# Performance work log

Measured on AMD Instinct MI355X. Metric: run time of the kernel, lower is better.

The kernel has to match this reference:

```python
import jax, jax.numpy as jnp
import numpy as np

N, E, B, T, F, H, O = 50000, 800000, 16, 4, 128, 128, 128
LEAKY = 0.2  # PyG GATConv negative_slope default


def setup_inputs() -> dict:
    key = jax.random.key(0)
    ks = jax.random.split(key, 12)
    s = 0.05
    return {
        "x": jax.random.normal(ks[0], (T, N, F), jnp.float32),
        "edge_index": jax.random.randint(ks[1], (2, E), 0, N, dtype=jnp.int32),
        "batch_idx": jnp.sort(jax.random.randint(ks[2], (N,), 0, B, dtype=jnp.int32)),
        "W1": jax.random.normal(ks[3], (F, H), jnp.float32) * s,
        "att_src1": jax.random.normal(ks[4], (H,), jnp.float32) * s,
        "att_dst1": jax.random.normal(ks[5], (H,), jnp.float32) * s,
        "b1": jnp.zeros((H,), jnp.float32),
        "W2": jax.random.normal(ks[6], (H, O), jnp.float32) * s,
        "att_src2": jax.random.normal(ks[7], (O,), jnp.float32) * s,
        "att_dst2": jax.random.normal(ks[8], (O,), jnp.float32) * s,
        "b2": jnp.zeros((O,), jnp.float32),
    }


def gat_layer(h, src, dst, W, a_src, a_dst, b):
    # PyG GATConv, heads=1, concat=False, self-loops already appended.
    h = h @ W                                  # [N, out]
    alpha_s = h @ a_src                        # [N]
    alpha_d = h @ a_dst                        # [N]
    e = alpha_s[src] + alpha_d[dst]            # [E']
    e = jnp.where(e > 0, e, LEAKY * e)         # leaky_relu
    # softmax over incoming edges of each destination node (every node has a self-loop)
    m = jax.ops.segment_max(e, dst, num_segments=N)
    ex = jnp.exp(e - m[dst])
    z = jax.ops.segment_sum(ex, dst, num_segments=N)
    alpha = ex / z[dst]                        # [E']
    out = jax.ops.segment_sum(alpha[:, None] * h[src], dst, num_segments=N)
    return out + b


def reference(x, edge_index, batch_idx, W1, att_src1, att_dst1, b1, W2, att_src2, att_dst2, b2):
    loops = jnp.arange(N, dtype=edge_index.dtype)
    src = jnp.concatenate([edge_index[0], loops])  # add_self_loops (PyG default)
    dst = jnp.concatenate([edge_index[1], loops])
    ones = jnp.ones((N, 1), jnp.float32)
    cnt = jax.ops.segment_sum(ones, batch_idx, num_segments=B)  # [B,1]

    def per_snapshot(xt):
        h = gat_layer(xt, src, dst, W1, att_src1, att_dst1, b1)
        h = jax.nn.relu(h)                     # inter-layer ReLU (dropout=0, eval)
        h = gat_layer(h, src, dst, W2, att_src2, att_dst2, b2)
        return jax.ops.segment_sum(h, batch_idx, num_segments=B) / cnt  # mean pool [B,O]

    reps = jax.vmap(per_snapshot)(x)           # [T, B, O]
    return jnp.transpose(reps, (1, 0, 2))      # [B, T, O]
```

## Files before the change

kernel.cpp:

```cpp
#include <hip/hip_runtime.h>
#include <hip/hip_bf16.h>

#define LEAKY 0.2f

typedef __attribute__((ext_vector_type(8))) short bf16x8;
typedef __attribute__((ext_vector_type(4))) float f32x4;
typedef __attribute__((ext_vector_type(2))) float f32x2;


__global__ __launch_bounds__(256) void k_init(int* cnt, int* bstart, int* hist, int n, int nb) {
    int i = blockIdx.x * 256 + threadIdx.x;
    if (i < n) cnt[i] = 1;
    if (i < nb) bstart[i] = n;
    if (i < 32) hist[i] = 0;
}

__global__ __launch_bounds__(256) void k_count(const int* __restrict__ dst, int* cnt, int e,
                                               const int* __restrict__ bidx, int* bstart, int n) {
    int i = blockIdx.x * 256 + threadIdx.x;
    if (i < e) atomicAdd(&cnt[dst[i]], 1);
    if (i < n) {
        int b = bidx[i];
        if (i == 0 || bidx[i - 1] != b) atomicMin(&bstart[b], i);
    }
}

__device__ inline int block_incl_scan(int v, int* lds) {
    int lane = threadIdx.x & 63, wid = threadIdx.x >> 6;
    int s = v;
#pragma unroll
    for (int o = 1; o < 64; o <<= 1) { int t = __shfl_up(s, o); if (lane >= o) s += t; }
    if (lane == 63) lds[wid] = s;
    __syncthreads();
    int add = 0;
#pragma unroll
    for (int ww = 0; ww < 3; ++ww) if (ww < wid) add += lds[ww];
    return s + add;
}

__global__ __launch_bounds__(256) void k_scanA(const int* __restrict__ cnt, int* bsum, int n) {
    __shared__ int lds[4];
    int i = blockIdx.x * 256 + threadIdx.x;
    int v = (i < n) ? ((cnt[i] + 7) & ~7) : 0;
    int s = block_incl_scan(v, lds);
    if (threadIdx.x == 255) bsum[blockIdx.x] = s;
}

__global__ __launch_bounds__(256) void k_scanB(int* bsum, int* boff, int nb,
                                               int* bstart, int n, int nbatch) {
    __shared__ int lds[4];
    int i = threadIdx.x;
    int v = (i < nb) ? bsum[i] : 0;
    int s = block_incl_scan(v, lds);
    if (i < nb) boff[i] = s - v;
    if (i == 0) {
        bstart[nbatch] = n;
        for (int b = nbatch - 1; b >= 0; --b)
            if (bstart[b] == n) bstart[b] = bstart[b + 1];
    }
}

__global__ __launch_bounds__(256) void k_scanC(const int* __restrict__ cnt, const int* __restrict__ boff,
                                               int* row_ptr, int* csr, int* cursor, int* hist, int n) {
    __shared__ int lds[4];
    __shared__ int lh[32];
    int tid = threadIdx.x;
    if (tid < 32) lh[tid] = 0;
    int i = blockIdx.x * 256 + tid;
    int v = (i < n) ? ((cnt[i] + 7) & ~7) : 0;
    int s = block_incl_scan(v, lds) + boff[blockIdx.x];
    __syncthreads();
    if (i < n) {
        int excl = s - v;
        row_ptr[i + 1] = s;
        csr[excl] = i;
        cursor[i] = excl + 1;
        atomicAdd(&lh[min(v >> 3, 31)], 1);
    }
    if (i == 0) row_ptr[0] = 0;
    __syncthreads();
    if (tid < 32 && lh[tid]) atomicAdd(&hist[tid], lh[tid]);
}

__global__ __launch_bounds__(256) void k_scatter(const int* __restrict__ src, const int* __restrict__ dst,
                                                 int* cursor, int* csr, int e) {
    int i = blockIdx.x * 256 + threadIdx.x;
    if (i < e) { int p = atomicAdd(&cursor[dst[i]], 1); csr[p] = src[i]; }
}

__global__ void k_bscan(const int* __restrict__ hist, int* bcur) {
    int run = 0;
    for (int b = 0; b < 32; ++b) { bcur[b] = run; run += hist[b]; }
}

__global__ __launch_bounds__(256) void k_pad(const int* __restrict__ row_ptr, const int* __restrict__ cursor,
                                             int* csr, int* bcur, int* perm, int n) {
    __shared__ int lh[32];
    __shared__ int lbase[32];
    int tid = threadIdx.x;
    if (tid < 32) lh[tid] = 0;
    __syncthreads();
    int i = blockIdx.x * 256 + tid;
    int bkt = 0, lpos = 0, b0 = 0, p = 0, e = 0;
    if (i < n) {
        b0 = row_ptr[i]; p = cursor[i]; e = row_ptr[i + 1];
        bkt = min((e - b0) >> 3, 31);
        lpos = atomicAdd(&lh[bkt], 1);
    }
    __syncthreads();
    if (tid < 32 && lh[tid]) lbase[tid] = atomicAdd(&bcur[tid], lh[tid]);
    __syncthreads();
    if (i < n) {
        perm[lbase[bkt] + lpos] = i;
        int v = i | 0x80000000;
        for (; p < e; ++p) csr[p] = v;
    }
}

__device__ inline unsigned short bf16r(float x) {
    unsigned int u = __float_as_uint(x);
    u += 0x7fffu + ((u >> 16) & 1u);
    return (unsigned short)(u >> 16);
}

__device__ inline unsigned int bfpair(float lo, float hi) {
    unsigned int ul = __float_as_uint(lo); ul += 0x7fffu + ((ul >> 16) & 1u);
    unsigned int uh = __float_as_uint(hi); uh += 0x7fffu + ((uh >> 16) & 1u);
    return (ul >> 16) | (uh & 0xffff0000u);
}

__global__ __launch_bounds__(256) void k_prep(const float* __restrict__ W1, unsigned short* __restrict__ wt1g,
                                              const float* __restrict__ W2, unsigned short* __restrict__ wt2g) {
    int bi = blockIdx.x;
    const float* W = (bi < 64) ? W1 : W2;
    unsigned short* wtg = (bi < 64) ? wt1g : wt2g;
    int idx = (bi & 63) * 256 + threadIdx.x;
    int k = idx >> 7, n = idx & 127;
    int kg = k >> 3, kr = k & 7;
    wtg[(n * 16 + (kg ^ (n & 15))) * 8 + kr] = bf16r(W[k * 128 + n]);
}

template <bool ABF16>
__global__ __launch_bounds__(256) void k_gemm_mfma(
    const void* __restrict__ Asrc, const unsigned short* __restrict__ wtg,
    const float* __restrict__ asrc, const float* __restrict__ adst,
    unsigned char* __restrict__ hq, float* __restrict__ vas, float* __restrict__ vad,
    int nrows)
{
    __shared__ unsigned short Wt[128 * 128];
    int tid = threadIdx.x;
    int lane = tid & 63, wv = tid >> 6;
    int row0 = blockIdx.x * 64;
    int c0 = lane & 15, g = lane >> 4;

    int rA = min(row0 + wv * 16 + c0, nrows - 1);

    bf16x8 af[4];
    uint4 stg[8];
    {
        const uint4* s4 = (const uint4*)wtg;
#pragma unroll
        for (int i = 0; i < 8; ++i) stg[i] = s4[tid + i * 256];
    }
    if (ABF16) {
#pragma unroll
        for (int ks = 0; ks < 4; ++ks)
            af[ks] = *(const bf16x8*)((const unsigned short*)Asrc + (size_t)rA * 128 + ks * 32 + g * 8);
    } else {
        float4 raw[4][2];
#pragma unroll
        for (int ks = 0; ks < 4; ++ks) {
            const float4* ap = (const float4*)((const float*)Asrc + (size_t)rA * 128 + ks * 32 + g * 8);
            raw[ks][0] = ap[0];
            raw[ks][1] = ap[1];
        }
#pragma unroll
        for (int ks = 0; ks < 4; ++ks) {
            float4 f0 = raw[ks][0], f1 = raw[ks][1];
            uint4 p = make_uint4(bfpair(f0.x, f0.y), bfpair(f0.z, f0.w),
                                 bfpair(f1.x, f1.y), bfpair(f1.z, f1.w));
            af[ks] = *(bf16x8*)&p;
        }
    }
    {
        uint4* d4 = (uint4*)Wt;
#pragma unroll
        for (int i = 0; i < 8; ++i) d4[tid + i * 256] = stg[i];
    }
    __syncthreads();

    f32x4 acc[8];
#pragma unroll
    for (int ni = 0; ni < 8; ++ni)
#pragma unroll
        for (int q = 0; q < 4; ++q) acc[ni][q] = 0.f;

#pragma unroll
    for (int ks = 0; ks < 4; ++ks) {
        int kgbase = ks * 4;
        bf16x8 bfr[8];
#pragma unroll
        for (int ni = 0; ni < 8; ++ni) {
            int n = ni * 16 + c0;
            bfr[ni] = *(const bf16x8*)&Wt[(n * 16 + ((kgbase + g) ^ c0)) * 8];
        }
#pragma unroll
        for (int ni = 0; ni < 8; ++ni)
            acc[ni] = __builtin_amdgcn_mfma_f32_16x16x32_bf16(bfr[ni], af[ks], acc[ni], 0, 0, 0);
    }

    float4 as4[8], ad4[8];
#pragma unroll
    for (int ni = 0; ni < 8; ++ni) {
        as4[ni] = *(const float4*)&asrc[ni * 16 + g * 4];
        ad4[ni] = *(const float4*)&adst[ni * 16 + g * 4];
    }
    {
        int node = row0 + wv * 16 + c0;
        bool ok = node < nrows;
        float s = 0.f, d = 0.f;
        unsigned packs[8];
#pragma unroll
        for (int ni = 0; ni < 8; ++ni) {
            f32x4 vv = acc[ni];
            s = fmaf(vv[0], as4[ni].x, fmaf(vv[1], as4[ni].y, fmaf(vv[2], as4[ni].z, fmaf(vv[3], as4[ni].w, s))));
            d = fmaf(vv[0], ad4[ni].x, fmaf(vv[1], ad4[ni].y, fmaf(vv[2], ad4[ni].z, fmaf(vv[3], ad4[ni].w, d))));
            unsigned p0 = (unsigned)__builtin_amdgcn_cvt_pk_fp8_f32(vv[0], vv[1], 0, false);
            packs[ni] = (unsigned)__builtin_amdgcn_cvt_pk_fp8_f32(vv[2], vv[3], (int)p0, true);
        }
        s += __shfl_xor(s, 16); s += __shfl_xor(s, 32);
        d += __shfl_xor(d, 16); d += __shfl_xor(d, 32);
        if (ok) {
            if (g == 0) { vas[node] = s; vad[node] = d; }
#pragma unroll
            for (int ni = 0; ni < 8; ++ni)
                *(unsigned*)&hq[(size_t)node * 128 + ni * 16 + g * 4] = packs[ni];
        }
    }
}

template <bool RELU>
__global__ __launch_bounds__(256) void k_agg(const unsigned char* __restrict__ hq,
                                             const float* __restrict__ vas,
                                             const float* __restrict__ vad,
                                             const int* __restrict__ row_ptr,
                                             const int* __restrict__ csr,
                                             const int* __restrict__ perm,
                                             const float* __restrict__ bias,
                                             unsigned int* __restrict__ outb,
                                             int n, int chunksPerT) {
    int i = blockIdx.x;
    int slot = i & 7;
    int t = slot >> 1;
    int chunk = ((i >> 3) << 1) | (slot & 1);
    if (chunk >= chunksPerT) return;
    int tid = threadIdx.x;
    int grp = tid >> 3, l = tid & 7;
    int idx = chunk * 32 + grp;
    if (idx >= n) return;
    int w = perm[idx];
    unsigned int tbase = (unsigned int)t * (unsigned int)n;
    unsigned int g = tbase + (unsigned int)w;
    int beg = row_ptr[w], end = row_ptr[w + 1];
    float advl = vad[g];

    f32x2 acc2[8];
#pragma unroll
    for (int q = 0; q < 8; ++q) { acc2[q].x = 0.f; acc2[q].y = 0.f; }
    float zp = 0.f;

    for (int c = beg; c < end; c += 8) {
        int raw = csr[c + l];
        unsigned int s_l = tbase + (unsigned int)(raw & 0x7fffffff);
        float e = vas[s_l] + advl;
        e = e > 0.f ? e : LEAKY * e;
        float w_l = (raw >= 0) ? __expf(e) : 0.f;
        zp += w_l;

        unsigned int ofs[8]; float wt[8];
#pragma unroll
        for (int q = 0; q < 8; ++q) {
            ofs[q] = __shfl(s_l, q, 8) * 128u + (unsigned int)(l * 16);
            wt[q] = __shfl(w_l, q, 8);
        }
        uint4 v[8];
#pragma unroll
        for (int q = 0; q < 8; ++q)
            v[q] = *(const uint4*)&hq[ofs[q]];
#pragma unroll
        for (int q = 0; q < 8; ++q) {
            f32x2 w2; w2.x = wt[q]; w2.y = wt[q];
            acc2[0] = __builtin_elementwise_fma(w2, __builtin_amdgcn_cvt_pk_f32_fp8(v[q].x, false), acc2[0]);
            acc2[1] = __builtin_elementwise_fma(w2, __builtin_amdgcn_cvt_pk_f32_fp8(v[q].x, true),  acc2[1]);
            acc2[2] = __builtin_elementwise_fma(w2, __builtin_amdgcn_cvt_pk_f32_fp8(v[q].y, false), acc2[2]);
            acc2[3] = __builtin_elementwise_fma(w2, __builtin_amdgcn_cvt_pk_f32_fp8(v[q].y, true),  acc2[3]);
            acc2[4] = __builtin_elementwise_fma(w2, __builtin_amdgcn_cvt_pk_f32_fp8(v[q].z, false), acc2[4]);
            acc2[5] = __builtin_elementwise_fma(w2, __builtin_amdgcn_cvt_pk_f32_fp8(v[q].z, true),  acc2[5]);
            acc2[6] = __builtin_elementwise_fma(w2, __builtin_amdgcn_cvt_pk_f32_fp8(v[q].w, false), acc2[6]);
            acc2[7] = __builtin_elementwise_fma(w2, __builtin_amdgcn_cvt_pk_f32_fp8(v[q].w, true),  acc2[7]);
        }
    }

    float z = zp;
    z += __shfl_xor(z, 1, 8);
    z += __shfl_xor(z, 2, 8);
    z += __shfl_xor(z, 4, 8);
    float inv = 1.0f / z;

    const float4* bias4 = (const float4*)&bias[l * 16];
    unsigned u[8];
#pragma unroll
    for (int j = 0; j < 4; ++j) {
        float4 bb = bias4[j];
        float o0 = fmaf(acc2[2 * j].x, inv, bb.x);
        float o1 = fmaf(acc2[2 * j].y, inv, bb.y);
        float o2 = fmaf(acc2[2 * j + 1].x, inv, bb.z);
        float o3 = fmaf(acc2[2 * j + 1].y, inv, bb.w);
        if (RELU) {
            o0 = fmaxf(o0, 0.f); o1 = fmaxf(o1, 0.f); o2 = fmaxf(o2, 0.f); o3 = fmaxf(o3, 0.f);
        }
        u[2 * j]     = bfpair(o0, o1);
        u[2 * j + 1] = bfpair(o2, o3);
    }
    *(uint4*)&outb[(size_t)g * 64 + l * 8]     = make_uint4(u[0], u[1], u[2], u[3]);
    *(uint4*)&outb[(size_t)g * 64 + l * 8 + 4] = make_uint4(u[4], u[5], u[6], u[7]);
}

__global__ __launch_bounds__(128) void k_pool(const unsigned int* __restrict__ h,
                                              const int* __restrict__ bstart,
                                              float* __restrict__ out, int n, int T) {
    int b = blockIdx.x;
    int chunk = blockIdx.y;
    int t = blockIdx.z;
    int f = threadIdx.x;
    int s = bstart[b], e = bstart[b + 1];
    int cnt = e - s;
    if (cnt <= 0) return;
    int len = (cnt + 31) / 32;
    int cs = s + chunk * len;
    int ce = min(cs + len, e);
    if (cs >= ce) return;
    const unsigned int* ht = h + (size_t)t * n * 64;
    float acc = 0.f;
    for (int nidx = cs; nidx < ce; ++nidx) {
        unsigned int v = ht[(size_t)nidx * 64 + (f >> 1)];
        acc += __uint_as_float((f & 1) ? (v & 0xffff0000u) : (v << 16));
    }
    atomicAdd(&out[(size_t)(b * T + t) * 128 + f], acc / (float)cnt);
}


extern "C" void kernel_launch(void* const* d_in, const int* in_sizes, int n_in,
                              void* d_out, int out_size, void* d_ws, size_t ws_size,
                              hipStream_t stream) {
    const float* x    = (const float*)d_in[0];
    const int*   ei   = (const int*)d_in[1];
    const int*   bidx = (const int*)d_in[2];
    const float* W1   = (const float*)d_in[3];
    const float* as1  = (const float*)d_in[4];
    const float* ad1  = (const float*)d_in[5];
    const float* b1   = (const float*)d_in[6];
    const float* W2   = (const float*)d_in[7];
    const float* as2  = (const float*)d_in[8];
    const float* ad2  = (const float*)d_in[9];
    const float* b2   = (const float*)d_in[10];
    float* out = (float*)d_out;

    const int E = in_sizes[1] / 2;
    const int N = in_sizes[2];
    const int T = in_sizes[0] / (N * 128);
    const int B = out_size / (T * 128);
    const int* src = ei;
    const int* dst = ei + E;
    const int NT = N * T;

    char* wsp = (char*)d_ws;
    auto alloc = [&](size_t bytes) { void* p = wsp; wsp += (bytes + 255) / 256 * 256; return p; };
    unsigned char* hq    = (unsigned char*)alloc((size_t)NT * 128);
    unsigned int* hb2    = (unsigned int*)alloc((size_t)NT * 64 * 4);
    float* vas           = (float*)alloc((size_t)NT * 4);
    float* vad           = (float*)alloc((size_t)NT * 4);
    unsigned short* wt1g = (unsigned short*)alloc(128 * 128 * 2);
    unsigned short* wt2g = (unsigned short*)alloc(128 * 128 * 2);
    int* row_ptr         = (int*)alloc((size_t)(N + 1) * 4);
    int* cnt             = (int*)alloc((size_t)N * 4);
    int* csr             = (int*)alloc(((size_t)E + 16ull * N + 64) * 4);
    int* perm            = (int*)alloc((size_t)N * 4);
    int* hist            = (int*)alloc(32 * 4);
    int* bcur            = (int*)alloc(32 * 4);
    int* bstart          = (int*)alloc((size_t)(B + 2) * 4);
    int  nScanB          = (N + 255) / 256;
    int* bsum            = (int*)alloc((size_t)nScanB * 4);
    int* boff            = (int*)alloc((size_t)nScanB * 4);

    hipMemsetAsync(d_out, 0, (size_t)out_size * sizeof(float), stream);

    int gN = (N + 255) / 256, gE = (E + 255) / 256;
    k_init<<<gN, 256, 0, stream>>>(cnt, bstart, hist, N, B + 1);
    k_count<<<gE, 256, 0, stream>>>(dst, cnt, E, bidx, bstart, N);
    k_prep<<<128, 256, 0, stream>>>(W1, wt1g, W2, wt2g);
    k_scanA<<<nScanB, 256, 0, stream>>>(cnt, bsum, N);
    k_scanB<<<1, 256, 0, stream>>>(bsum, boff, nScanB, bstart, N, B);
    k_scanC<<<nScanB, 256, 0, stream>>>(cnt, boff, row_ptr, csr, cnt, hist, N);
    k_scatter<<<gE, 256, 0, stream>>>(src, dst, cnt, csr, E);
    k_bscan<<<1, 1, 0, stream>>>(hist, bcur);
    k_pad<<<gN, 256, 0, stream>>>(row_ptr, cnt, csr, bcur, perm, N);

    int gGemm = (NT + 63) / 64;
    int chunksPerT = (N + 31) / 32;
    int chunksPad = ((chunksPerT + 1) / 2) * 2;
    int gAggFlat = chunksPad * 4;
    k_gemm_mfma<false><<<gGemm, 256, 0, stream>>>(x,   wt1g, as1, ad1, hq, vas, vad, NT);
    k_agg<true ><<<gAggFlat, 256, 0, stream>>>(hq, vas, vad, row_ptr, csr, perm, b1, hb2, N, chunksPerT);
    k_gemm_mfma<true ><<<gGemm, 256, 0, stream>>>(hb2, wt2g, as2, ad2, hq, vas, vad, NT);
    k_agg<false><<<gAggFlat, 256, 0, stream>>>(hq, vas, vad, row_ptr, csr, perm, b2, hb2, N, chunksPerT);
    k_pool<<<dim3(B, 32, T), 128, 0, stream>>>(hb2, bstart, out, N, T);
}
```

Baseline: 323.6 us.

## Make GEMM kernel persistent with software-prefetched A tiles

The projection GEMM kernel becomes persistent: the grid is capped at 1024 blocks, each block loads the 32KB transposed weight into shared memory once and loops over 64-row tiles with a grid stride. The A-row loads for the next tile are issued before the MFMA work on the current tile, so global latency overlaps compute. This removes the per-block cost of reloading the weight tile (NT/64 ≈ 3125 blocks before) at the price of more live registers, which may lower occupancy.

```diff
diff --git a/kernel.cpp b/kernel.cpp
--- a/kernel.cpp
+++ b/kernel.cpp
@@ -145,68 +145,18 @@
     const void* __restrict__ Asrc, const unsigned short* __restrict__ wtg,
     const float* __restrict__ asrc, const float* __restrict__ adst,
     unsigned char* __restrict__ hq, float* __restrict__ vas, float* __restrict__ vad,
-    int nrows)
+    int nrows, int nTiles)
 {
     __shared__ unsigned short Wt[128 * 128];
     int tid = threadIdx.x;
     int lane = tid & 63, wv = tid >> 6;
-    int row0 = blockIdx.x * 64;
     int c0 = lane & 15, g = lane >> 4;
 
-    int rA = min(row0 + wv * 16 + c0, nrows - 1);
-
-    bf16x8 af[4];
-    uint4 stg[8];
     {
         const uint4* s4 = (const uint4*)wtg;
-#pragma unroll
-        for (int i = 0; i < 8; ++i) stg[i] = s4[tid + i * 256];
-    }
-    if (ABF16) {
-#pragma unroll
-        for (int ks = 0; ks < 4; ++ks)
-            af[ks] = *(const bf16x8*)((const unsigned short*)Asrc + (size_t)rA * 128 + ks * 32 + g * 8);
-    } else {
-        float4 raw[4][2];
-#pragma unroll
-        for (int ks = 0; ks < 4; ++ks) {
-            const float4* ap = (const float4*)((const float*)Asrc + (size_t)rA * 128 + ks * 32 + g * 8);
-            raw[ks][0] = ap[0];
-            raw[ks][1] = ap[1];
-        }
-#pragma unroll
-        for (int ks = 0; ks < 4; ++ks) {
-            float4 f0 = raw[ks][0], f1 = raw[ks][1];
-            uint4 p = make_uint4(bfpair(f0.x, f0.y), bfpair(f0.z, f0.w),
-                                 bfpair(f1.x, f1.y), bfpair(f1.z, f1.w));
-            af[ks] = *(bf16x8*)&p;
-        }
-    }
-    {
         uint4* d4 = (uint4*)Wt;
 #pragma unroll
-        for (int i = 0; i < 8; ++i) d4[tid + i * 256] = stg[i];
-    }
-    __syncthreads();
-
-    f32x4 acc[8];
-#pragma unroll
-    for (int ni = 0; ni < 8; ++ni)
-#pragma unroll
-        for (int q = 0; q < 4; ++q) acc[ni][q] = 0.f;
-
-#pragma unroll
-    for (int ks = 0; ks < 4; ++ks) {
-        int kgbase = ks * 4;
-        bf16x8 bfr[8];
-#pragma unroll
-        for (int ni = 0; ni < 8; ++ni) {
-            int n = ni * 16 + c0;
-            bfr[ni] = *(const bf16x8*)&Wt[(n * 16 + ((kgbase + g) ^ c0)) * 8];
-        }
-#pragma unroll
-        for (int ni = 0; ni < 8; ++ni)
-            acc[ni] = __builtin_amdgcn_mfma_f32_16x16x32_bf16(bfr[ni], af[ks], acc[ni], 0, 0, 0);
+        for (int i = 0; i < 8; ++i) d4[tid + i * 256] = s4[tid + i * 256];
     }
 
     float4 as4[8], ad4[8];
@@ -215,27 +165,108 @@
         as4[ni] = *(const float4*)&asrc[ni * 16 + g * 4];
         ad4[ni] = *(const float4*)&adst[ni * 16 + g * 4];
     }
+
+    int tile = blockIdx.x;
+    if (tile >= nTiles) { __syncthreads(); return; }
+
+    bf16x8 af[4];
+    float4 raw[4][2];
     {
-        int node = row0 + wv * 16 + c0;
-        bool ok = node < nrows;
-        float s = 0.f, d = 0.f;
-        unsigned packs[8];
-#pragma unroll
-        for (int ni = 0; ni < 8; ++ni) {
-            f32x4 vv = acc[ni];
-            s = fmaf(vv[0], as4[ni].x, fmaf(vv[1], as4[ni].y, fmaf(vv[2], as4[ni].z, fmaf(vv[3], as4[ni].w, s))));
-            d = fmaf(vv[0], ad4[ni].x, fmaf(vv[1], ad4[ni].y, fmaf(vv[2], ad4[ni].z, fmaf(vv[3], ad4[ni].w, d))));
-            unsigned p0 = (unsigned)__builtin_amdgcn_cvt_pk_fp8_f32(vv[0], vv[1], 0, false);
-            packs[ni] = (unsigned)__builtin_amdgcn_cvt_pk_fp8_f32(vv[2], vv[3], (int)p0, true);
-        }
-        s += __shfl_xor(s, 16); s += __shfl_xor(s, 32);
-        d += __shfl_xor(d, 16); d += __shfl_xor(d, 32);
-        if (ok) {
-            if (g == 0) { vas[node] = s; vad[node] = d; }
+        int rA = min(tile * 64 + wv * 16 + c0, nrows - 1);
+        if (ABF16) {
+#pragma unroll
+            for (int ks = 0; ks < 4; ++ks)
+                af[ks] = *(const bf16x8*)((const unsigned short*)Asrc + (size_t)rA * 128 + ks * 32 + g * 8);
+        } else {
+#pragma unroll
+            for (int ks = 0; ks < 4; ++ks) {
+                const float4* ap = (const float4*)((const float*)Asrc + (size_t)rA * 128 + ks * 32 + g * 8);
+                raw[ks][0] = ap[0];
+                raw[ks][1] = ap[1];
+            }
+        }
+    }
+    __syncthreads();
+
+    while (tile < nTiles) {
+        int nextTile = tile + gridDim.x;
+        if (!ABF16) {
+#pragma unroll
+            for (int ks = 0; ks < 4; ++ks) {
+                float4 f0 = raw[ks][0], f1 = raw[ks][1];
+                uint4 p = make_uint4(bfpair(f0.x, f0.y), bfpair(f0.z, f0.w),
+                                     bfpair(f1.x, f1.y), bfpair(f1.z, f1.w));
+                af[ks] = *(bf16x8*)&p;
+            }
+        }
+        bf16x8 afn[4];
+        float4 rawn[4][2];
+        if (nextTile < nTiles) {
+            int rA = min(nextTile * 64 + wv * 16 + c0, nrows - 1);
+            if (ABF16) {
+#pragma unroll
+                for (int ks = 0; ks < 4; ++ks)
+                    afn[ks] = *(const bf16x8*)((const unsigned short*)Asrc + (size_t)rA * 128 + ks * 32 + g * 8);
+            } else {
+#pragma unroll
+                for (int ks = 0; ks < 4; ++ks) {
+                    const float4* ap = (const float4*)((const float*)Asrc + (size_t)rA * 128 + ks * 32 + g * 8);
+                    rawn[ks][0] = ap[0];
+                    rawn[ks][1] = ap[1];
+                }
+            }
+        }
+
+        f32x4 acc[8];
+#pragma unroll
+        for (int ni = 0; ni < 8; ++ni)
+#pragma unroll
+            for (int q = 0; q < 4; ++q) acc[ni][q] = 0.f;
+#pragma unroll
+        for (int ks = 0; ks < 4; ++ks) {
+            int kgbase = ks * 4;
+            bf16x8 bfr[8];
+#pragma unroll
+            for (int ni = 0; ni < 8; ++ni) {
+                int n = ni * 16 + c0;
+                bfr[ni] = *(const bf16x8*)&Wt[(n * 16 + ((kgbase + g) ^ c0)) * 8];
+            }
 #pragma unroll
             for (int ni = 0; ni < 8; ++ni)
-                *(unsigned*)&hq[(size_t)node * 128 + ni * 16 + g * 4] = packs[ni];
-        }
+                acc[ni] = __builtin_amdgcn_mfma_f32_16x16x32_bf16(bfr[ni], af[ks], acc[ni], 0, 0, 0);
+        }
+
+        {
+            int node = tile * 64 + wv * 16 + c0;
+            bool ok = node < nrows;
+            float s = 0.f, d = 0.f;
+            unsigned packs[8];
+#pragma unroll
+            for (int ni = 0; ni < 8; ++ni) {
+                f32x4 vv = acc[ni];
+                s = fmaf(vv[0], as4[ni].x, fmaf(vv[1], as4[ni].y, fmaf(vv[2], as4[ni].z, fmaf(vv[3], as4[ni].w, s))));
+                d = fmaf(vv[0], ad4[ni].x, fmaf(vv[1], ad4[ni].y, fmaf(vv[2], ad4[ni].z, fmaf(vv[3], ad4[ni].w, d))));
+                unsigned p0 = (unsigned)__builtin_amdgcn_cvt_pk_fp8_f32(vv[0], vv[1], 0, false);
+                packs[ni] = (unsigned)__builtin_amdgcn_cvt_pk_fp8_f32(vv[2], vv[3], (int)p0, true);
+            }
+            s += __shfl_xor(s, 16); s += __shfl_xor(s, 32);
+            d += __shfl_xor(d, 16); d += __shfl_xor(d, 32);
+            if (ok) {
+                if (g == 0) { vas[node] = s; vad[node] = d; }
+#pragma unroll
+                for (int ni = 0; ni < 8; ++ni)
+                    *(unsigned*)&hq[(size_t)node * 128 + ni * 16 + g * 4] = packs[ni];
+            }
+        }
+
+        if (ABF16) {
+#pragma unroll
+            for (int ks = 0; ks < 4; ++ks) af[ks] = afn[ks];
+        } else {
+#pragma unroll
+            for (int ks = 0; ks < 4; ++ks) { raw[ks][0] = rawn[ks][0]; raw[ks][1] = rawn[ks][1]; }
+        }
+        tile = nextTile;
     }
 }
 
@@ -406,13 +437,14 @@
     k_bscan<<<1, 1, 0, stream>>>(hist, bcur);
     k_pad<<<gN, 256, 0, stream>>>(row_ptr, cnt, csr, bcur, perm, N);
 
-    int gGemm = (NT + 63) / 64;
+    int nTiles = (NT + 63) / 64;
+    int gGemm = min(nTiles, 1024);
     int chunksPerT = (N + 31) / 32;
     int chunksPad = ((chunksPerT + 1) / 2) * 2;
     int gAggFlat = chunksPad * 4;
-    k_gemm_mfma<false><<<gGemm, 256, 0, stream>>>(x,   wt1g, as1, ad1, hq, vas, vad, NT);
+    k_gemm_mfma<false><<<gGemm, 256, 0, stream>>>(x,   wt1g, as1, ad1, hq, vas, vad, NT, nTiles);
     k_agg<true ><<<gAggFlat, 256, 0, stream>>>(hq, vas, vad, row_ptr, csr, perm, b1, hb2, N, chunksPerT);
-    k_gemm_mfma<true ><<<gGemm, 256, 0, stream>>>(hb2, wt2g, as2, ad2, hq, vas, vad, NT);
+    k_gemm_mfma<true ><<<gGemm, 256, 0, stream>>>(hb2, wt2g, as2, ad2, hq, vas, vad, NT, nTiles);
     k_agg<false><<<gAggFlat, 256, 0, stream>>>(hq, vas, vad, row_ptr, csr, perm, b2, hb2, N, chunksPerT);
     k_pool<<<dim3(B, 32, T), 128, 0, stream>>>(hb2, bstart, out, N, T);
 }
```

After: 324.3 us. Within noise of the previous version (+0.2%).
